# Kernel optimization log

Measured on AMD Instinct MI355X. Metric: run time of the kernel, lower is better.

## Reference

```python
import jax, jax.numpy as jnp
import numpy as np

N, E, F_IN, H, K = 100000, 1600000, 256, 128, 5


def setup_inputs() -> dict:
    key = jax.random.key(0)
    ks = jax.random.split(key, 24)

    def rn(k, shape, scale=0.05):
        return jax.random.normal(k, shape, dtype=jnp.float32) * scale

    inp = {
        "x": rn(ks[0], (N, F_IN), 1.0),
        "edge_index": jax.random.randint(ks[1], (2, E), 0, N, dtype=jnp.int64),
        "edge_attr": jax.random.uniform(ks[2], (N, K), dtype=jnp.float32),
        "pre_W": rn(ks[3], (F_IN, H)),
        "pre_b": jnp.zeros((H,), jnp.float32),
        "c1_Ws": rn(ks[4], (H, H)),
        "c1_Wn": rn(ks[5], (H, H)),
        "c1_b": jnp.zeros((H,), jnp.float32),
        "c2_Ws": rn(ks[6], (H, H)),
        "c2_Wn": rn(ks[7], (H, H)),
        "c2_b": jnp.zeros((H,), jnp.float32),
        "nodepost_W": rn(ks[8], (H, H)),
        "nodepost_b": jnp.zeros((H,), jnp.float32),
        "d_W0": rn(ks[9], (K, H)),
        "d_b0": jnp.zeros((H,), jnp.float32),
        "d_W1": rn(ks[10], (H, H)),
        "d_b1": jnp.zeros((H,), jnp.float32),
        "d_W2": rn(ks[11], (H, H)),
        "d_b2": jnp.zeros((H,), jnp.float32),
        "d_W3": rn(ks[12], (H, H)),
        "d_b3": jnp.zeros((H,), jnp.float32),
        "final_W": rn(ks[13], (2 * H, 1)),
        "final_b": jnp.zeros((1,), jnp.float32),
    }
    return inp


def _mean_agg(h, src, dst, n):
    # scatter-mean of source features onto destination nodes
    s = jax.ops.segment_sum(h[src], dst, num_segments=n)  # [N, H]
    deg = jax.ops.segment_sum(jnp.ones_like(dst, dtype=h.dtype), dst, num_segments=n)
    return s / jnp.maximum(deg, 1.0)[:, None]


def reference(x, edge_index, edge_attr, pre_W, pre_b,
              c1_Ws, c1_Wn, c1_b, c2_Ws, c2_Wn, c2_b,
              nodepost_W, nodepost_b,
              d_W0, d_b0, d_W1, d_b1, d_W2, d_b2, d_W3, d_b3,
              final_W, final_b):
    n = x.shape[0]
    src, dst = edge_index[0], edge_index[1]

    # --- feat path: NodeAttributeAggregator ---
    h = x @ pre_W + pre_b                                   # pre_process_mlp
    agg = _mean_agg(h, src, dst, n)
    h = jax.nn.relu(h @ c1_Ws + agg @ c1_Wn + c1_b)          # layer1 conv + act
    agg = _mean_agg(h, src, dst, n)
    h = jax.nn.relu(h @ c2_Ws + agg @ c2_Wn + c2_b)          # layer2 conv + act
    feat_out = h @ nodepost_W + nodepost_b                   # post_process_mlp

    # --- dist path: EdgeAttributeAggregator (MLP over edge attrs) ---
    e = edge_attr.reshape(-1, K)
    y = jax.nn.relu(e @ d_W0 + d_b0)
    y = jax.nn.relu(y @ d_W1 + d_b1)
    y = jax.nn.relu(y @ d_W2 + d_b2)
    dist_out = y @ d_W3 + d_b3

    # --- merge 'cat' + final MLP + squeeze + sigmoid ---
    z = jnp.concatenate([feat_out, dist_out], axis=1)        # [N, 2H]
    out = (z @ final_W + final_b).squeeze(1)                  # [N]
    return jax.nn.sigmoid(out)
```

## Files before the change

kernel.cpp:

```cpp
#include <hip/hip_runtime.h>

#define HF 128
#define CAP 64
#define PSHIFT 17
#define BUCKET_BLOCKS 2048

typedef __attribute__((ext_vector_type(8))) short s16x8;
typedef __attribute__((ext_vector_type(4))) float f32x4;
typedef __attribute__((ext_vector_type(2))) float f32x2;

__device__ __forceinline__ unsigned short f2bf(float f) {
    unsigned u = __float_as_uint(f);
    return (unsigned short)((u + 0x7fff + ((u >> 16) & 1)) >> 16);
}

#if __has_builtin(__builtin_amdgcn_cvt_pk_fp8_f32) && __has_builtin(__builtin_amdgcn_cvt_pk_f32_fp8)
#define FP8_HW 1
#else
#define FP8_HW 0
#endif

__device__ __forceinline__ unsigned char f2fp8(float f) {
#if FP8_HW
    int v = __builtin_amdgcn_cvt_pk_fp8_f32(f, f, 0, false);
    return (unsigned char)(v & 0xff);
#else
    unsigned u = __float_as_uint(f);
    unsigned s = (u >> 24) & 0x80;
    float a = fabsf(f);
    if (a > 448.f) a = 448.f;
    if (a < 0.015625f) {
        int q = (int)(a * 512.f + 0.5f);
        return (unsigned char)(s | q);
    }
    unsigned ub = __float_as_uint(a);
    ub += 0x0007ffff + ((ub >> 20) & 1);
    int e8 = (int)(ub >> 23) - 127 + 7;
    if (e8 >= 16) return (unsigned char)(s | 0x7e);
    return (unsigned char)(s | (e8 << 3) | ((ub >> 20) & 7));
#endif
}

__device__ __forceinline__ void fp8acc4(unsigned w, float* acc) {
#if FP8_HW
    f32x2 lo = __builtin_amdgcn_cvt_pk_f32_fp8(w, false);
    f32x2 hi = __builtin_amdgcn_cvt_pk_f32_fp8(w, true);
    acc[0] += lo.x; acc[1] += lo.y; acc[2] += hi.x; acc[3] += hi.y;
#else
    #pragma unroll
    for (int j = 0; j < 4; ++j) {
        unsigned b = (w >> (8 * j)) & 0xff;
        unsigned s = (b >> 7) & 1, e = (b >> 3) & 15, m = b & 7;
        float v = e ? __uint_as_float(((e + 120) << 23) | (m << 20))
                    : (float)m * 0.001953125f;
        acc[j] += s ? -v : v;
    }
#endif
}

__device__ __forceinline__ void repack_one(
    const float* __restrict__ W, short* __restrict__ Wp, int K, int t)
{
    int nkt = K >> 5;
    int lane = t & 63;
    int kt = (t >> 6) % nkt;
    int nt = (t >> 6) / nkt;
    int c = nt * 16 + (lane & 15);
    int kbase = kt * 32 + (lane >> 4) * 8;
    s16x8 v;
    #pragma unroll
    for (int j = 0; j < 8; ++j) v[j] = (short)f2bf(W[(long)(kbase + j) * HF + c]);
    *(s16x8*)(Wp + (long)t * 8) = v;
}

__global__ __launch_bounds__(256) void repack_all(
    const float* __restrict__ preW, const float* __restrict__ c1Ws,
    const float* __restrict__ c1Wn, const float* __restrict__ c2Ws,
    const float* __restrict__ c2Wn, const float* __restrict__ dW1,
    const float* __restrict__ dW2,
    short* preWp, short* c1Wsp, short* c1Wnp, short* c2Wsp, short* c2Wnp,
    short* dW1p, short* dW2p,
    const float* __restrict__ npW, const float* __restrict__ npb,
    const float* __restrict__ dW3, const float* __restrict__ db3,
    const float* __restrict__ fW,  const float* __restrict__ fb,
    float* __restrict__ uvc)
{
    int b = blockIdx.x;
    if (b == 64) {
        int i = threadIdx.x;
        if (i < HF) {
            float u = 0.f, v = 0.f;
            for (int j = 0; j < HF; ++j) {
                u += npW[i * HF + j] * fW[j];
                v += dW3[i * HF + j] * fW[HF + j];
            }
            uvc[i] = u;
            uvc[HF + i] = v;
            if (i == 0) {
                float c = fb[0];
                for (int j = 0; j < HF; ++j) c += npb[j] * fW[j] + db3[j] * fW[HF + j];
                uvc[2 * HF] = c;
            }
        }
        return;
    }
    if (b < 16) { repack_one(preW, preWp, 256, b * 256 + threadIdx.x); return; }
    int m = (b - 16) >> 3, t = ((b - 16) & 7) * 256 + threadIdx.x;
    const float* W; short* Wp;
    switch (m) {
        case 0: W = c1Ws; Wp = c1Wsp; break;
        case 1: W = c1Wn; Wp = c1Wnp; break;
        case 2: W = c2Ws; Wp = c2Wsp; break;
        case 3: W = c2Wn; Wp = c2Wnp; break;
        case 4: W = dW1;  Wp = dW1p;  break;
        default: W = dW2; Wp = dW2p;  break;
    }
    repack_one(W, Wp, HF, t);
}

__global__ __launch_bounds__(256) void bucketx_kernel(
    const int* __restrict__ eidx, long E,
    int* __restrict__ deg, int* __restrict__ bucket, int npass)
{
    const int xcd   = blockIdx.x & 7;
    const int chunk = blockIdx.x >> 3;
    const int nchunks = BUCKET_BLOCKS / 8;
    long per = (E + nchunks - 1) / nchunks;
    per = (per + 3) & ~3L;
    const long e0 = (long)chunk * per;
    const long e1 = (e0 + per < E) ? e0 + per : E;
    if (e0 >= E) return;
    for (int p = 0; p < npass; ++p) {
        for (long e = e0 + (long)threadIdx.x * 4; e + 4 <= e1; e += 1024) {
            int4 d4 = *(const int4*)(eidx + E + e);
            #pragma unroll
            for (int j = 0; j < 4; ++j) {
                int d = (&d4.x)[j];
                if ((d >> PSHIFT) != p || ((d >> 4) & 7) != xcd) continue;
                int s = eidx[e + j];
                int pos = atomicAdd(&deg[d], 1);
                if (pos < CAP) bucket[(long)d * CAP + pos] = s;
            }
        }
        for (long e = (e1 & ~3L) + threadIdx.x; e < e1; e += 256) {
            int d = eidx[E + e];
            if ((d >> PSHIFT) != p || ((d >> 4) & 7) != xcd) continue;
            int s = eidx[e];
            int pos = atomicAdd(&deg[d], 1);
            if (pos < CAP) bucket[(long)d * CAP + pos] = s;
        }
    }
}

__device__ __forceinline__ void agg_tile512(
    const unsigned char* __restrict__ hq, const int* __restrict__ deg,
    const int* __restrict__ bucket, int n, long row0B, int wv, int lane,
    unsigned* lds)
{
    const int g = lane >> 4;
    const int i = lane & 15;
    #pragma unroll
    for (int it = 0; it < 2; ++it) {
        const int rl = wv * 8 + it * 4 + g;
        const long node = row0B + rl;
        float acc[8];
        #pragma unroll
        for (int j = 0; j < 8; ++j) acc[j] = 0.f;
        int dg = 0, m = 0;
        const int* bl = bucket;
        if (node < n) {
            dg = deg[node];
            m = dg < CAP ? dg : CAP;
            bl = bucket + node * CAP;
        }
        int e = 0;
        for (; e + 8 <= m; e += 8) {
            int4 sa = *(const int4*)(bl + e);
            int4 sb = *(const int4*)(bl + e + 4);
            uint2 v0 = *(const uint2*)(hq + (long)sa.x * HF + i * 8);
            uint2 v1 = *(const uint2*)(hq + (long)sa.y * HF + i * 8);
            uint2 v2 = *(const uint2*)(hq + (long)sa.z * HF + i * 8);
            uint2 v3 = *(const uint2*)(hq + (long)sa.w * HF + i * 8);
            uint2 v4 = *(const uint2*)(hq + (long)sb.x * HF + i * 8);
            uint2 v5 = *(const uint2*)(hq + (long)sb.y * HF + i * 8);
            uint2 v6 = *(const uint2*)(hq + (long)sb.z * HF + i * 8);
            uint2 v7 = *(const uint2*)(hq + (long)sb.w * HF + i * 8);
            fp8acc4(v0.x, acc); fp8acc4(v0.y, acc + 4);
            fp8acc4(v1.x, acc); fp8acc4(v1.y, acc + 4);
            fp8acc4(v2.x, acc); fp8acc4(v2.y, acc + 4);
            fp8acc4(v3.x, acc); fp8acc4(v3.y, acc + 4);
            fp8acc4(v4.x, acc); fp8acc4(v4.y, acc + 4);
            fp8acc4(v5.x, acc); fp8acc4(v5.y, acc + 4);
            fp8acc4(v6.x, acc); fp8acc4(v6.y, acc + 4);
            fp8acc4(v7.x, acc); fp8acc4(v7.y, acc + 4);
        }
        for (; e + 4 <= m; e += 4) {
            int4 sa = *(const int4*)(bl + e);
            uint2 v0 = *(const uint2*)(hq + (long)sa.x * HF + i * 8);
            uint2 v1 = *(const uint2*)(hq + (long)sa.y * HF + i * 8);
            uint2 v2 = *(const uint2*)(hq + (long)sa.z * HF + i * 8);
            uint2 v3 = *(const uint2*)(hq + (long)sa.w * HF + i * 8);
            fp8acc4(v0.x, acc); fp8acc4(v0.y, acc + 4);
            fp8acc4(v1.x, acc); fp8acc4(v1.y, acc + 4);
            fp8acc4(v2.x, acc); fp8acc4(v2.y, acc + 4);
            fp8acc4(v3.x, acc); fp8acc4(v3.y, acc + 4);
        }
        for (; e < m; ++e) {
            uint2 v = *(const uint2*)(hq + (long)bl[e] * HF + i * 8);
            fp8acc4(v.x, acc); fp8acc4(v.y, acc + 4);
        }
        const float sc = 1.f / (float)(dg > 1 ? dg : 1);
        uint4 o;
        o.x = (unsigned)f2bf(acc[0] * sc) | ((unsigned)f2bf(acc[1] * sc) << 16);
        o.y = (unsigned)f2bf(acc[2] * sc) | ((unsigned)f2bf(acc[3] * sc) << 16);
        o.z = (unsigned)f2bf(acc[4] * sc) | ((unsigned)f2bf(acc[5] * sc) << 16);
        o.w = (unsigned)f2bf(acc[6] * sc) | ((unsigned)f2bf(acc[7] * sc) << 16);
        *(uint4*)&lds[rl * 64 + ((i ^ (rl & 15)) << 2)] = o;
    }
}

__device__ __forceinline__ void gemm_pass4(
    const unsigned short* __restrict__ Av, const short* __restrict__ Wp,
    long rA, int lane, int nb, f32x4 acc[4])
{
    const int q = lane >> 4;
    #pragma unroll
    for (int kt = 0; kt < 4; ++kt) {
        s16x8 a = *(const s16x8*)(Av + rA * HF + kt * 32 + q * 8);
        #pragma unroll
        for (int j = 0; j < 4; ++j) {
            s16x8 b = *(const s16x8*)(Wp + ((long)((nb + j) * 4 + kt) * 64 + lane) * 8);
            acc[j] = __builtin_amdgcn_mfma_f32_16x16x32_bf16(a, b, acc[j], 0, 0, 0);
        }
    }
}

__device__ __forceinline__ void gemm_pass_lds4(
    const unsigned* lds, int w3, int lane, const short* __restrict__ Wp,
    int nb, f32x4 acc[4])
{
    const int q = lane >> 4;
    const int i15 = lane & 15;
    const int rl = w3 * 16 + i15;
    #pragma unroll
    for (int kt = 0; kt < 4; ++kt) {
        s16x8 a = *(const s16x8*)&lds[rl * 64 + (((kt * 4 + q) ^ i15) << 2)];
        #pragma unroll
        for (int j = 0; j < 4; ++j) {
            s16x8 b = *(const s16x8*)(Wp + ((long)((nb + j) * 4 + kt) * 64 + lane) * 8);
            acc[j] = __builtin_amdgcn_mfma_f32_16x16x32_bf16(a, b, acc[j], 0, 0, 0);
        }
    }
}

__device__ __forceinline__ void gemm_pass_mfma8(
    const unsigned short* __restrict__ Av, const short* __restrict__ Wp,
    long rA, int lane, f32x4 acc[8])
{
    const int q = lane >> 4;
    #pragma unroll
    for (int kt = 0; kt < 4; ++kt) {
        s16x8 a = *(const s16x8*)(Av + rA * HF + kt * 32 + q * 8);
        #pragma unroll
        for (int nt = 0; nt < 8; ++nt) {
            s16x8 b = *(const s16x8*)(Wp + ((long)(nt * 4 + kt) * 64 + lane) * 8);
            acc[nt] = __builtin_amdgcn_mfma_f32_16x16x32_bf16(a, b, acc[nt], 0, 0, 0);
        }
    }
}

__device__ __forceinline__ void gemm_pass_lds8(
    const unsigned* lds, int w3, int lane, const short* __restrict__ Wp, f32x4 acc[8])
{
    const int q = lane >> 4;
    const int i15 = lane & 15;
    const int rl = w3 * 16 + i15;
    #pragma unroll
    for (int kt = 0; kt < 4; ++kt) {
        s16x8 a = *(const s16x8*)&lds[rl * 64 + (((kt * 4 + q) ^ i15) << 2)];
        #pragma unroll
        for (int nt = 0; nt < 8; ++nt) {
            s16x8 b = *(const s16x8*)(Wp + ((long)(nt * 4 + kt) * 64 + lane) * 8);
            acc[nt] = __builtin_amdgcn_mfma_f32_16x16x32_bf16(a, b, acc[nt], 0, 0, 0);
        }
    }
}

__global__ __launch_bounds__(512) void megapd_kernel(
    const float* __restrict__ x, const short* __restrict__ preWp,
    const float* __restrict__ preb, unsigned short* __restrict__ h0,
    unsigned char* __restrict__ h0q,
    const float* __restrict__ ea, const float* __restrict__ W0,
    const float* __restrict__ b0, const short* __restrict__ W1p,
    const float* __restrict__ b1, unsigned short* __restrict__ y1,
    int n, int gemmBlocks)
{
    __shared__ unsigned ldsx[64 * 128];
    const int lane = threadIdx.x & 63;
    const int wv   = threadIdx.x >> 6;
    const int w3   = wv & 3;
    const int nb   = (wv >> 2) * 4;

    if (blockIdx.x < gemmBlocks) {
        const long row0B = (long)blockIdx.x * 64;
        {
            const int t = threadIdx.x;
            const int row = t >> 3;
            const int c0 = (t & 7) * 32;
            long rr = row0B + row;
            if (rr > n - 1) rr = n - 1;
            const float* xp = x + rr * 256 + c0;
            unsigned pk[16];
            #pragma unroll
            for (int k = 0; k < 8; ++k) {
                float4 f = *(const float4*)(xp + k * 4);
                pk[2 * k]     = (unsigned)f2bf(f.x) | ((unsigned)f2bf(f.y) << 16);
                pk[2 * k + 1] = (unsigned)f2bf(f.z) | ((unsigned)f2bf(f.w) << 16);
            }
            #pragma unroll
            for (int k = 0; k < 4; ++k) {
                int c = (t & 7) * 4 + k;
                int phys = c ^ (row & 31);
                *(uint4*)&ldsx[row * 128 + phys * 4] =
                    make_uint4(pk[4 * k], pk[4 * k + 1], pk[4 * k + 2], pk[4 * k + 3]);
            }
        }
        __syncthreads();

        f32x4 acc[4];
        #pragma unroll
        for (int j = 0; j < 4; ++j)
            #pragma unroll
            for (int i = 0; i < 4; ++i) acc[j][i] = 0.f;

        const int rl = w3 * 16 + (lane & 15);
        const int q = lane >> 4;
        #pragma unroll
        for (int kt = 0; kt < 8; ++kt) {
            int c = kt * 4 + q;
            s16x8 a = *(const s16x8*)&ldsx[rl * 128 + ((c ^ (rl & 31)) << 2)];
            #pragma unroll
            for (int j = 0; j < 4; ++j) {
                s16x8 b = *(const s16x8*)(preWp + ((long)((nb + j) * 8 + kt) * 64 + lane) * 8);
                acc[j] = __builtin_amdgcn_mfma_f32_16x16x32_bf16(a, b, acc[j], 0, 0, 0);
            }
        }

        const long row0 = row0B + w3 * 16;
        const int cq = lane >> 4;
        #pragma unroll
        for (int j = 0; j < 4; ++j) {
            int col = (nb + j) * 16 + (lane & 15);
            float bs = preb[col];
            #pragma unroll
            for (int i = 0; i < 4; ++i) {
                long r = row0 + cq * 4 + i;
                if (r < n) {
                    float o = acc[j][i] + bs;
                    h0[r * HF + col] = f2bf(o);
                    h0q[r * HF + col] = f2fp8(o);
                }
            }
        }
    } else {
        const long row0 = (long)(blockIdx.x - gemmBlocks) * 64 + w3 * 16;
        const int q = lane >> 4;
        long rA = row0 + (lane & 15);
        if (rA > n - 1) rA = n - 1;

        float e0 = ea[rA * 5 + 0], e1 = ea[rA * 5 + 1], e2 = ea[rA * 5 + 2],
              e3 = ea[rA * 5 + 3], e4 = ea[rA * 5 + 4];

        f32x4 acc[4];
        #pragma unroll
        for (int j = 0; j < 4; ++j)
            #pragma unroll
            for (int i = 0; i < 4; ++i) acc[j][i] = 0.f;

        #pragma unroll
        for (int kt = 0; kt < 4; ++kt) {
            const int c = kt * 32 + q * 8;
            s16x8 a;
            #pragma unroll
            for (int h = 0; h < 2; ++h) {
                float4 w0 = *(const float4*)(W0 + 0 * HF + c + h * 4);
                float4 w1 = *(const float4*)(W0 + 1 * HF + c + h * 4);
                float4 w2 = *(const float4*)(W0 + 2 * HF + c + h * 4);
                float4 w3v = *(const float4*)(W0 + 3 * HF + c + h * 4);
                float4 w4 = *(const float4*)(W0 + 4 * HF + c + h * 4);
                float4 bb = *(const float4*)(b0 + c + h * 4);
                float z0 = fmaxf(bb.x + e0 * w0.x + e1 * w1.x + e2 * w2.x + e3 * w3v.x + e4 * w4.x, 0.f);
                float z1 = fmaxf(bb.y + e0 * w0.y + e1 * w1.y + e2 * w2.y + e3 * w3v.y + e4 * w4.y, 0.f);
                float z2 = fmaxf(bb.z + e0 * w0.z + e1 * w1.z + e2 * w2.z + e3 * w3v.z + e4 * w4.z, 0.f);
                float z3 = fmaxf(bb.w + e0 * w0.w + e1 * w1.w + e2 * w2.w + e3 * w3v.w + e4 * w4.w, 0.f);
                a[h * 4 + 0] = (short)f2bf(z0); a[h * 4 + 1] = (short)f2bf(z1);
                a[h * 4 + 2] = (short)f2bf(z2); a[h * 4 + 3] = (short)f2bf(z3);
            }
            #pragma unroll
            for (int j = 0; j < 4; ++j) {
                s16x8 b = *(const s16x8*)(W1p + ((long)((nb + j) * 4 + kt) * 64 + lane) * 8);
                acc[j] = __builtin_amdgcn_mfma_f32_16x16x32_bf16(a, b, acc[j], 0, 0, 0);
            }
        }

        const int cq = lane >> 4;
        #pragma unroll
        for (int j = 0; j < 4; ++j) {
            int col = (nb + j) * 16 + (lane & 15);
            float bs = b1[col];
            #pragma unroll
            for (int i = 0; i < 4; ++i) {
                long r = row0 + cq * 4 + i;
                if (r < n) y1[r * HF + col] = f2bf(fmaxf(acc[j][i] + bs, 0.f));
            }
        }
    }
}

__global__ __launch_bounds__(512) void c1f_kernel(
    const unsigned short* __restrict__ h0, const unsigned char* __restrict__ h0q,
    const int* __restrict__ deg, const int* __restrict__ bucket,
    const short* __restrict__ Wsp, const short* __restrict__ Wnp,
    const float* __restrict__ bias, unsigned short* __restrict__ out,
    unsigned char* __restrict__ outq, int n)
{
    __shared__ unsigned ldsagg[64 * 64];
    const int lane = threadIdx.x & 63;
    const int wv   = threadIdx.x >> 6;
    const long row0B = (long)blockIdx.x * 64;

    agg_tile512(h0q, deg, bucket, n, row0B, wv, lane, ldsagg);
    __syncthreads();

    const int w3 = wv & 3;
    const int nb = (wv >> 2) * 4;

    f32x4 acc[4];
    #pragma unroll
    for (int j = 0; j < 4; ++j)
        #pragma unroll
        for (int i = 0; i < 4; ++i) acc[j][i] = 0.f;

    const long row0 = row0B + w3 * 16;
    long rA = row0 + (lane & 15);
    if (rA > n - 1) rA = n - 1;

    gemm_pass4(h0, Wsp, rA, lane, nb, acc);
    gemm_pass_lds4(ldsagg, w3, lane, Wnp, nb, acc);

    const int cq = lane >> 4;
    #pragma unroll
    for (int j = 0; j < 4; ++j) {
        int col = (nb + j) * 16 + (lane & 15);
        float bs = bias[col];
        #pragma unroll
        for (int i = 0; i < 4; ++i) {
            long r = row0 + cq * 4 + i;
            if (r < n) {
                float o = fmaxf(acc[j][i] + bs, 0.f);
                out[r * HF + col] = f2bf(o);
                outq[r * HF + col] = f2fp8(o);
            }
        }
    }
}

__global__ __launch_bounds__(512) void tailf_kernel(
    const unsigned short* __restrict__ h1, const unsigned char* __restrict__ h1q,
    const unsigned short* __restrict__ y1,
    const int* __restrict__ deg, const int* __restrict__ bucket,
    const short* __restrict__ c2Wsp, const short* __restrict__ c2Wnp,
    const short* __restrict__ dW2p,
    const float* __restrict__ c2b, const float* __restrict__ db2,
    const float* __restrict__ uvc, float* __restrict__ out, int n)
{
    __shared__ unsigned ldsagg[64 * 64];
    __shared__ float pp[2][64];
    const int lane = threadIdx.x & 63;
    const int wv   = threadIdx.x >> 6;
    const long row0B = (long)blockIdx.x * 64;

    agg_tile512(h1q, deg, bucket, n, row0B, wv, lane, ldsagg);
    __syncthreads();

    const int w = wv & 3;
    const long row0 = row0B + w * 16;
    long rA = row0 + (lane & 15);
    if (rA > n - 1) rA = n - 1;
    const int cq = lane >> 4;
    float part[4] = {0.f, 0.f, 0.f, 0.f};

    f32x4 acc[8];
    #pragma unroll
    for (int nt = 0; nt < 8; ++nt)
        #pragma unroll
        for (int i = 0; i < 4; ++i) acc[nt][i] = 0.f;

    if (wv < 4) {
        gemm_pass_mfma8(h1, c2Wsp, rA, lane, acc);
        gemm_pass_lds8(ldsagg, w, lane, c2Wnp, acc);
        #pragma unroll
        for (int nt = 0; nt < 8; ++nt) {
            int col = nt * 16 + (lane & 15);
            float bh = c2b[col], uu = uvc[col];
            #pragma unroll
            for (int i = 0; i < 4; ++i)
                part[i] += fmaxf(acc[nt][i] + bh, 0.f) * uu;
        }
    } else {
        gemm_pass_mfma8(y1, dW2p, rA, lane, acc);
        #pragma unroll
        for (int nt = 0; nt < 8; ++nt) {
            int col = nt * 16 + (lane & 15);
            float by = db2[col], vv = uvc[HF + col];
            #pragma unroll
            for (int i = 0; i < 4; ++i)
                part[i] += fmaxf(acc[nt][i] + by, 0.f) * vv;
        }
    }

    #pragma unroll
    for (int i = 0; i < 4; ++i) {
        float s = part[i];
        s += __shfl_xor(s, 1, 64);
        s += __shfl_xor(s, 2, 64);
        s += __shfl_xor(s, 4, 64);
        s += __shfl_xor(s, 8, 64);
        part[i] = s;
    }
    if ((lane & 15) == 0) {
        #pragma unroll
        for (int i = 0; i < 4; ++i)
            pp[wv >> 2][w * 16 + cq * 4 + i] = part[i];
    }
    __syncthreads();

    if (threadIdx.x < 64) {
        long r = row0B + threadIdx.x;
        if (r < n) {
            float s = pp[0][threadIdx.x] + pp[1][threadIdx.x] + uvc[2 * HF];
            out[r] = 1.f / (1.f + expf(-s));
        }
    }
}

extern "C" void kernel_launch(void* const* d_in, const int* in_sizes, int n_in,
                              void* d_out, int out_size, void* d_ws, size_t ws_size,
                              hipStream_t stream)
{
    const float* x      = (const float*)d_in[0];
    const int*   eidx   = (const int*)  d_in[1];
    const float* eattr  = (const float*)d_in[2];
    const float* pre_W  = (const float*)d_in[3];
    const float* pre_b  = (const float*)d_in[4];
    const float* c1_Ws  = (const float*)d_in[5];
    const float* c1_Wn  = (const float*)d_in[6];
    const float* c1_b   = (const float*)d_in[7];
    const float* c2_Ws  = (const float*)d_in[8];
    const float* c2_Wn  = (const float*)d_in[9];
    const float* c2_b   = (const float*)d_in[10];
    const float* npW    = (const float*)d_in[11];
    const float* npb    = (const float*)d_in[12];
    const float* dW0    = (const float*)d_in[13];
    const float* db0    = (const float*)d_in[14];
    const float* dW1    = (const float*)d_in[15];
    const float* db1    = (const float*)d_in[16];
    const float* dW2    = (const float*)d_in[17];
    const float* db2    = (const float*)d_in[18];
    const float* dW3    = (const float*)d_in[19];
    const float* db3    = (const float*)d_in[20];
    const float* fW     = (const float*)d_in[21];
    const float* fb     = (const float*)d_in[22];

    const int  n = in_sizes[0] / 256;
    const long E = in_sizes[1] / 2;

    char* ws = (char*)d_ws;
    size_t off = 0;
    auto alloc = [&](size_t bytes) -> void* {
        void* p = ws + off;
        off += (bytes + 255) & ~(size_t)255;
        return p;
    };
    unsigned short* B0 = (unsigned short*)alloc((size_t)n * HF * 2);
    unsigned short* B1 = (unsigned short*)alloc((size_t)n * HF * 2);
    unsigned short* B2 = (unsigned short*)alloc((size_t)n * HF * 2);
    unsigned char*  B0q = (unsigned char*)alloc((size_t)n * HF);
    unsigned char*  B1q = (unsigned char*)alloc((size_t)n * HF);
    int*   deg    = (int*)alloc((size_t)n * sizeof(int));
    int*   bucket = (int*)alloc((size_t)n * CAP * sizeof(int));
    float* uvc    = (float*)alloc((2 * HF + 1) * sizeof(float));
    short* preWp  = (short*)alloc(256 * HF * 2);
    short* c1Wsp  = (short*)alloc(HF * HF * 2);
    short* c1Wnp  = (short*)alloc(HF * HF * 2);
    short* c2Wsp  = (short*)alloc(HF * HF * 2);
    short* c2Wnp  = (short*)alloc(HF * HF * 2);
    short* dW1p   = (short*)alloc(HF * HF * 2);
    short* dW2p   = (short*)alloc(HF * HF * 2);

    const int gemmBlocks = (n + 63) / 64;
    const int npass = ((n - 1) >> PSHIFT) + 1;

    repack_all<<<65, 256, 0, stream>>>(
        pre_W, c1_Ws, c1_Wn, c2_Ws, c2_Wn, dW1, dW2,
        preWp, c1Wsp, c1Wnp, c2Wsp, c2Wnp, dW1p, dW2p,
        npW, npb, dW3, db3, fW, fb, uvc);

    hipMemsetAsync(deg, 0, (size_t)n * sizeof(int), stream);

    bucketx_kernel<<<BUCKET_BLOCKS, 256, 0, stream>>>(eidx, E, deg, bucket, npass);

    megapd_kernel<<<2 * gemmBlocks, 512, 0, stream>>>(
        x, preWp, pre_b, B0, B0q,
        eattr, dW0, db0, dW1p, db1, B2,
        n, gemmBlocks);

    c1f_kernel<<<gemmBlocks, 512, 0, stream>>>(
        B0, B0q, deg, bucket, c1Wsp, c1Wnp, c1_b, B1, B1q, n);

    tailf_kernel<<<gemmBlocks, 512, 0, stream>>>(
        B1, B1q, B2, deg, bucket, c2Wsp, c2Wnp, dW2p, c2_b, db2, uvc, (float*)d_out, n);
}
```

Baseline: 316.1 us.

## Split fused pre/dist kernel, load x via global_load_lds, coalesce output stores through LDS

Splits the combined pre-process and distance-head kernel into two separate launches. The pre-process GEMM now copies fp32 x rows straight into swizzled LDS with global_load_lds and converts to bf16 at fragment-read time. Both kernels stage results in LDS and write 16-byte coalesced rows, replacing the scattered 2-byte and 1-byte stores. This aims to cut global-store inefficiency and load latency, at the cost of an extra launch, losing the overlap of the two halves, and a 64KB LDS footprint that may reduce occupancy.

```diff
diff --git a/kernel.cpp b/kernel.cpp
--- a/kernel.cpp
+++ b/kernel.cpp
@@ -286,134 +286,166 @@
     }
 }
 
-__global__ __launch_bounds__(512) void megapd_kernel(
+__global__ __launch_bounds__(512) void prek_kernel(
     const float* __restrict__ x, const short* __restrict__ preWp,
     const float* __restrict__ preb, unsigned short* __restrict__ h0,
-    unsigned char* __restrict__ h0q,
+    unsigned char* __restrict__ h0q, int n)
+{
+    __shared__ float ldsx[64 * 256];
+    const int lane = threadIdx.x & 63;
+    const int wv   = threadIdx.x >> 6;
+    const long row0B = (long)blockIdx.x * 64;
+
+    #pragma unroll
+    for (int rr = 0; rr < 8; ++rr) {
+        const int row = wv * 8 + rr;
+        const long gr = row0B + row;
+        if (gr < n) {
+            const int s = row & 7;
+            const float* gp = x + gr * 256 + ((lane ^ s) << 2);
+#if __has_builtin(__builtin_amdgcn_global_load_lds)
+            __builtin_amdgcn_global_load_lds(
+                (const __attribute__((address_space(1))) void*)gp,
+                (__attribute__((address_space(3))) void*)&ldsx[row * 256], 16, 0, 0);
+#else
+            float4 f = *(const float4*)gp;
+            *(float4*)&ldsx[row * 256 + lane * 4] = f;
+#endif
+        }
+    }
+    __syncthreads();
+
+    const int w3 = wv & 3;
+    const int nb = (wv >> 2) * 4;
+    const int q  = lane >> 4;
+    const int l15 = lane & 15;
+    const int rl = w3 * 16 + l15;
+    const int s  = rl & 7;
+
+    f32x4 acc[4];
+    #pragma unroll
+    for (int j = 0; j < 4; ++j)
+        #pragma unroll
+        for (int i = 0; i < 4; ++i) acc[j][i] = 0.f;
+
+    #pragma unroll
+    for (int kt = 0; kt < 8; ++kt) {
+        const int c0 = kt * 8 + q * 2;
+        float4 f0 = *(const float4*)&ldsx[rl * 256 + ((c0 ^ s) << 2)];
+        float4 f1 = *(const float4*)&ldsx[rl * 256 + (((c0 + 1) ^ s) << 2)];
+        s16x8 a;
+        a[0] = (short)f2bf(f0.x); a[1] = (short)f2bf(f0.y);
+        a[2] = (short)f2bf(f0.z); a[3] = (short)f2bf(f0.w);
+        a[4] = (short)f2bf(f1.x); a[5] = (short)f2bf(f1.y);
+        a[6] = (short)f2bf(f1.z); a[7] = (short)f2bf(f1.w);
+        #pragma unroll
+        for (int j = 0; j < 4; ++j) {
+            s16x8 b = *(const s16x8*)(preWp + ((long)((nb + j) * 8 + kt) * 64 + lane) * 8);
+            acc[j] = __builtin_amdgcn_mfma_f32_16x16x32_bf16(a, b, acc[j], 0, 0, 0);
+        }
+    }
+    __syncthreads();
+
+    unsigned short* lp16 = (unsigned short*)ldsx;
+    unsigned char*  lp8  = (unsigned char*)ldsx + 16384;
+    const int cq = lane >> 4;
+    #pragma unroll
+    for (int j = 0; j < 4; ++j) {
+        int col = (nb + j) * 16 + l15;
+        float bs = preb[col];
+        #pragma unroll
+        for (int i = 0; i < 4; ++i) {
+            int row = w3 * 16 + cq * 4 + i;
+            float o = acc[j][i] + bs;
+            lp16[row * 128 + col] = f2bf(o);
+            lp8[row * 128 + col]  = f2fp8(o);
+        }
+    }
+    __syncthreads();
+
+    const int r = threadIdx.x >> 3;
+    const int c = (threadIdx.x & 7) * 16;
+    const long gr = row0B + r;
+    if (gr < n) {
+        uint4* src = (uint4*)&lp16[r * 128 + c];
+        *(uint4*)(h0 + gr * HF + c)     = src[0];
+        *(uint4*)(h0 + gr * HF + c + 8) = src[1];
+        *(uint4*)(h0q + gr * HF + c)    = *(uint4*)&lp8[r * 128 + c];
+    }
+}
+
+__global__ __launch_bounds__(512) void disthead_kernel(
     const float* __restrict__ ea, const float* __restrict__ W0,
     const float* __restrict__ b0, const short* __restrict__ W1p,
-    const float* __restrict__ b1, unsigned short* __restrict__ y1,
-    int n, int gemmBlocks)
-{
-    __shared__ unsigned ldsx[64 * 128];
+    const float* __restrict__ b1, unsigned short* __restrict__ y1, int n)
+{
+    __shared__ unsigned short lpk[64 * 128];
     const int lane = threadIdx.x & 63;
     const int wv   = threadIdx.x >> 6;
     const int w3   = wv & 3;
     const int nb   = (wv >> 2) * 4;
-
-    if (blockIdx.x < gemmBlocks) {
-        const long row0B = (long)blockIdx.x * 64;
-        {
-            const int t = threadIdx.x;
-            const int row = t >> 3;
-            const int c0 = (t & 7) * 32;
-            long rr = row0B + row;
-            if (rr > n - 1) rr = n - 1;
-            const float* xp = x + rr * 256 + c0;
-            unsigned pk[16];
-            #pragma unroll
-            for (int k = 0; k < 8; ++k) {
-                float4 f = *(const float4*)(xp + k * 4);
-                pk[2 * k]     = (unsigned)f2bf(f.x) | ((unsigned)f2bf(f.y) << 16);
-                pk[2 * k + 1] = (unsigned)f2bf(f.z) | ((unsigned)f2bf(f.w) << 16);
-            }
-            #pragma unroll
-            for (int k = 0; k < 4; ++k) {
-                int c = (t & 7) * 4 + k;
-                int phys = c ^ (row & 31);
-                *(uint4*)&ldsx[row * 128 + phys * 4] =
-                    make_uint4(pk[4 * k], pk[4 * k + 1], pk[4 * k + 2], pk[4 * k + 3]);
-            }
-        }
-        __syncthreads();
-
-        f32x4 acc[4];
-        #pragma unroll
-        for (int j = 0; j < 4; ++j)
-            #pragma unroll
-            for (int i = 0; i < 4; ++i) acc[j][i] = 0.f;
-
-        const int rl = w3 * 16 + (lane & 15);
-        const int q = lane >> 4;
-        #pragma unroll
-        for (int kt = 0; kt < 8; ++kt) {
-            int c = kt * 4 + q;
-            s16x8 a = *(const s16x8*)&ldsx[rl * 128 + ((c ^ (rl & 31)) << 2)];
-            #pragma unroll
-            for (int j = 0; j < 4; ++j) {
-                s16x8 b = *(const s16x8*)(preWp + ((long)((nb + j) * 8 + kt) * 64 + lane) * 8);
-                acc[j] = __builtin_amdgcn_mfma_f32_16x16x32_bf16(a, b, acc[j], 0, 0, 0);
-            }
-        }
-
-        const long row0 = row0B + w3 * 16;
-        const int cq = lane >> 4;
+    const long row0B = (long)blockIdx.x * 64;
+    const long row0 = row0B + w3 * 16;
+    const int q = lane >> 4;
+    long rA = row0 + (lane & 15);
+    if (rA > n - 1) rA = n - 1;
+
+    float e0 = ea[rA * 5 + 0], e1 = ea[rA * 5 + 1], e2 = ea[rA * 5 + 2],
+          e3 = ea[rA * 5 + 3], e4 = ea[rA * 5 + 4];
+
+    f32x4 acc[4];
+    #pragma unroll
+    for (int j = 0; j < 4; ++j)
+        #pragma unroll
+        for (int i = 0; i < 4; ++i) acc[j][i] = 0.f;
+
+    #pragma unroll
+    for (int kt = 0; kt < 4; ++kt) {
+        const int c = kt * 32 + q * 8;
+        s16x8 a;
+        #pragma unroll
+        for (int h = 0; h < 2; ++h) {
+            float4 w0 = *(const float4*)(W0 + 0 * HF + c + h * 4);
+            float4 w1 = *(const float4*)(W0 + 1 * HF + c + h * 4);
+            float4 w2 = *(const float4*)(W0 + 2 * HF + c + h * 4);
+            float4 w3v = *(const float4*)(W0 + 3 * HF + c + h * 4);
+            float4 w4 = *(const float4*)(W0 + 4 * HF + c + h * 4);
+            float4 bb = *(const float4*)(b0 + c + h * 4);
+            float z0 = fmaxf(bb.x + e0 * w0.x + e1 * w1.x + e2 * w2.x + e3 * w3v.x + e4 * w4.x, 0.f);
+            float z1 = fmaxf(bb.y + e0 * w0.y + e1 * w1.y + e2 * w2.y + e3 * w3v.y + e4 * w4.y, 0.f);
+            float z2 = fmaxf(bb.z + e0 * w0.z + e1 * w1.z + e2 * w2.z + e3 * w3v.z + e4 * w4.z, 0.f);
+            float z3 = fmaxf(bb.w + e0 * w0.w + e1 * w1.w + e2 * w2.w + e3 * w3v.w + e4 * w4.w, 0.f);
+            a[h * 4 + 0] = (short)f2bf(z0); a[h * 4 + 1] = (short)f2bf(z1);
+            a[h * 4 + 2] = (short)f2bf(z2); a[h * 4 + 3] = (short)f2bf(z3);
+        }
         #pragma unroll
         for (int j = 0; j < 4; ++j) {
-            int col = (nb + j) * 16 + (lane & 15);
-            float bs = preb[col];
-            #pragma unroll
-            for (int i = 0; i < 4; ++i) {
-                long r = row0 + cq * 4 + i;
-                if (r < n) {
-                    float o = acc[j][i] + bs;
-                    h0[r * HF + col] = f2bf(o);
-                    h0q[r * HF + col] = f2fp8(o);
-                }
-            }
-        }
-    } else {
-        const long row0 = (long)(blockIdx.x - gemmBlocks) * 64 + w3 * 16;
-        const int q = lane >> 4;
-        long rA = row0 + (lane & 15);
-        if (rA > n - 1) rA = n - 1;
-
-        float e0 = ea[rA * 5 + 0], e1 = ea[rA * 5 + 1], e2 = ea[rA * 5 + 2],
-              e3 = ea[rA * 5 + 3], e4 = ea[rA * 5 + 4];
-
-        f32x4 acc[4];
-        #pragma unroll
-        for (int j = 0; j < 4; ++j)
-            #pragma unroll
-            for (int i = 0; i < 4; ++i) acc[j][i] = 0.f;
-
-        #pragma unroll
-        for (int kt = 0; kt < 4; ++kt) {
-            const int c = kt * 32 + q * 8;
-            s16x8 a;
-            #pragma unroll
-            for (int h = 0; h < 2; ++h) {
-                float4 w0 = *(const float4*)(W0 + 0 * HF + c + h * 4);
-                float4 w1 = *(const float4*)(W0 + 1 * HF + c + h * 4);
-                float4 w2 = *(const float4*)(W0 + 2 * HF + c + h * 4);
-                float4 w3v = *(const float4*)(W0 + 3 * HF + c + h * 4);
-                float4 w4 = *(const float4*)(W0 + 4 * HF + c + h * 4);
-                float4 bb = *(const float4*)(b0 + c + h * 4);
-                float z0 = fmaxf(bb.x + e0 * w0.x + e1 * w1.x + e2 * w2.x + e3 * w3v.x + e4 * w4.x, 0.f);
-                float z1 = fmaxf(bb.y + e0 * w0.y + e1 * w1.y + e2 * w2.y + e3 * w3v.y + e4 * w4.y, 0.f);
-                float z2 = fmaxf(bb.z + e0 * w0.z + e1 * w1.z + e2 * w2.z + e3 * w3v.z + e4 * w4.z, 0.f);
-                float z3 = fmaxf(bb.w + e0 * w0.w + e1 * w1.w + e2 * w2.w + e3 * w3v.w + e4 * w4.w, 0.f);
-                a[h * 4 + 0] = (short)f2bf(z0); a[h * 4 + 1] = (short)f2bf(z1);
-                a[h * 4 + 2] = (short)f2bf(z2); a[h * 4 + 3] = (short)f2bf(z3);
-            }
-            #pragma unroll
-            for (int j = 0; j < 4; ++j) {
-                s16x8 b = *(const s16x8*)(W1p + ((long)((nb + j) * 4 + kt) * 64 + lane) * 8);
-                acc[j] = __builtin_amdgcn_mfma_f32_16x16x32_bf16(a, b, acc[j], 0, 0, 0);
-            }
-        }
-
-        const int cq = lane >> 4;
-        #pragma unroll
-        for (int j = 0; j < 4; ++j) {
-            int col = (nb + j) * 16 + (lane & 15);
-            float bs = b1[col];
-            #pragma unroll
-            for (int i = 0; i < 4; ++i) {
-                long r = row0 + cq * 4 + i;
-                if (r < n) y1[r * HF + col] = f2bf(fmaxf(acc[j][i] + bs, 0.f));
-            }
-        }
+            s16x8 b = *(const s16x8*)(W1p + ((long)((nb + j) * 4 + kt) * 64 + lane) * 8);
+            acc[j] = __builtin_amdgcn_mfma_f32_16x16x32_bf16(a, b, acc[j], 0, 0, 0);
+        }
+    }
+
+    const int cq = lane >> 4;
+    const int l15 = lane & 15;
+    #pragma unroll
+    for (int j = 0; j < 4; ++j) {
+        int col = (nb + j) * 16 + l15;
+        float bs = b1[col];
+        #pragma unroll
+        for (int i = 0; i < 4; ++i) {
+            int row = w3 * 16 + cq * 4 + i;
+            lpk[row * 128 + col] = f2bf(fmaxf(acc[j][i] + bs, 0.f));
+        }
+    }
+    __syncthreads();
+
+    const int r = threadIdx.x >> 3;
+    const int c = (threadIdx.x & 7) * 16;
+    const long gr = row0B + r;
+    if (gr < n) {
+        uint4* src = (uint4*)&lpk[r * 128 + c];
+        *(uint4*)(y1 + gr * HF + c)     = src[0];
+        *(uint4*)(y1 + gr * HF + c + 8) = src[1];
     }
 }
 
@@ -610,10 +642,10 @@
 
     bucketx_kernel<<<BUCKET_BLOCKS, 256, 0, stream>>>(eidx, E, deg, bucket, npass);
 
-    megapd_kernel<<<2 * gemmBlocks, 512, 0, stream>>>(
-        x, preWp, pre_b, B0, B0q,
-        eattr, dW0, db0, dW1p, db1, B2,
-        n, gemmBlocks);
+    prek_kernel<<<gemmBlocks, 512, 0, stream>>>(x, preWp, pre_b, B0, B0q, n);
+
+    disthead_kernel<<<gemmBlocks, 512, 0, stream>>>(
+        eattr, dW0, db0, dW1p, db1, B2, n);
 
     c1f_kernel<<<gemmBlocks, 512, 0, stream>>>(
         B0, B0q, deg, bucket, c1Wsp, c1Wnp, c1_b, B1, B1q, n);
```

After: 315.1 us. Within noise of the previous version (-0.3%).
